# Kernel optimization log

Hardware: AMD Instinct MI355X
Metric: run time of the kernel (lower is better)

## Reference

```python
import math
import jax, jax.numpy as jnp
import numpy as np

HEADS = 20
NV = 6  # num_views


def _sdpa(q, k, v):
    # q,k,v: (B, H, Lq/Lk, D)
    d = q.shape[-1]
    scores = jnp.einsum('bhqd,bhkd->bhqk', q, k) * (1.0 / math.sqrt(d))
    return jnp.einsum('bhqk,bhkd->bhqd', jax.nn.softmax(scores, axis=-1), v)


def setup_inputs() -> dict:
    key = jax.random.key(0)
    ks = jax.random.split(key, 16)
    C = 1280
    bs, seq = 6, 1024
    w = 1.0 / math.sqrt(C)
    inp = {
        'hidden_states': jax.random.normal(ks[0], (bs, seq, C), jnp.float32),
        'ref_hidden_states': jax.random.normal(ks[1], (bs, seq, C), jnp.float32),
        'Wq': jax.random.normal(ks[2], (C, C), jnp.float32) * w,
        'Wk': jax.random.normal(ks[3], (C, C), jnp.float32) * w,
        'Wv': jax.random.normal(ks[4], (C, C), jnp.float32) * w,
        'Wout': jax.random.normal(ks[5], (C, C), jnp.float32) * w,
        'bout': jnp.zeros((C,), jnp.float32),
        'Wq_mv': jax.random.normal(ks[6], (C, C), jnp.float32) * w,
        'Wk_mv': jax.random.normal(ks[7], (C, C), jnp.float32) * w,
        'Wv_mv': jax.random.normal(ks[8], (C, C), jnp.float32) * w,
        'Wout_mv': jax.random.normal(ks[9], (C, C), jnp.float32) * w,
        'bout_mv': jnp.zeros((C,), jnp.float32),
        'Wq_ref': jax.random.normal(ks[10], (C, C), jnp.float32) * w,
        'Wk_ref': jax.random.normal(ks[11], (C, C), jnp.float32) * w,
        'Wv_ref': jax.random.normal(ks[12], (C, C), jnp.float32) * w,
        'Wout_ref': jax.random.normal(ks[13], (C, C), jnp.float32) * w,
        'bout_ref': jnp.zeros((C,), jnp.float32),
    }
    return inp


def reference(hidden_states, ref_hidden_states, Wq, Wk, Wv, Wout, bout,
              Wq_mv, Wk_mv, Wv_mv, Wout_mv, bout_mv,
              Wq_ref, Wk_ref, Wv_ref, Wout_ref, bout_ref):
    bs, seq, C = hidden_states.shape
    h = HEADS
    hd = Wq.shape[1] // h
    nv = NV
    b = bs // nv
    ih = iw = int(math.isqrt(seq))
    residual = hidden_states

    def split_heads(x):  # (bs, L, h*hd) -> (bs, h, L, hd)
        return x.reshape(bs, -1, h, hd).transpose(0, 2, 1, 3)

    def merge_heads(x):  # (bs, h, L, hd) -> (bs, L, h*hd)
        return x.transpose(0, 2, 1, 3).reshape(bs, -1, h * hd)

    # ---- base self-attention ----
    out = _sdpa(split_heads(hidden_states @ Wq),
                split_heads(hidden_states @ Wk),
                split_heads(hidden_states @ Wv))
    out = merge_heads(out) @ Wout + bout

    # ---- row-wise multi-view attention ----
    q_mv = (hidden_states @ Wq_mv).reshape(b, nv, ih, iw, h, hd)
    q_mv = q_mv.reshape(b * nv * ih, iw, h, hd).transpose(0, 2, 1, 3)  # (b*nv*ih, h, iw, hd)

    def mv_kv(x):
        # '(b nv)(ih iw) h c -> b ih (nv iw) h c', repeat_interleave(nv, dim=0)
        x = x.reshape(b, nv, ih, iw, h, hd).transpose(0, 2, 1, 3, 4, 5)
        x = x.reshape(b, ih, nv * iw, h, hd)
        x = jnp.repeat(x, nv, axis=0)  # (b*nv, ih, nv*iw, h, hd)
        return x.reshape(b * nv * ih, nv * iw, h, hd).transpose(0, 2, 1, 3)

    k_mv = mv_kv((hidden_states @ Wk_mv).reshape(bs, seq, h, hd).reshape(bs, seq, h * hd))
    v_mv = mv_kv((hidden_states @ Wv_mv))
    o_mv = _sdpa(q_mv, k_mv, v_mv)  # (b*nv*ih, h, iw, hd)
    # '(b nv ih) h iw c -> (b nv)(ih iw)(h c)'
    o_mv = o_mv.reshape(b, nv, ih, h, iw, hd).transpose(0, 1, 2, 4, 3, 5).reshape(bs, seq, h * hd)
    o_mv = o_mv @ Wout_mv + bout_mv

    # ---- reference image cross-attention ----
    o_ref = _sdpa(split_heads(hidden_states @ Wq_ref),
                  split_heads(ref_hidden_states @ Wk_ref),
                  split_heads(ref_hidden_states @ Wv_ref))
    o_ref = merge_heads(o_ref) @ Wout_ref + bout_ref

    mv_scale = 1.0
    ref_scale = 1.0
    return out + o_mv * mv_scale + o_ref * ref_scale + residual
```

## Files before the change

kernel.cpp:

```cpp
#include <hip/hip_runtime.h>
#include <hip/hip_bf16.h>


typedef __bf16 bf16;
typedef __bf16 bf16x8 __attribute__((ext_vector_type(8)));
typedef float f32x4 __attribute__((ext_vector_type(4)));

#define LOG2E 1.44269504088896340f

__device__ __forceinline__ unsigned pk2(float a, float b){
  unsigned short x = __builtin_bit_cast(unsigned short, (bf16)a);
  unsigned short y = __builtin_bit_cast(unsigned short, (bf16)b);
  return (unsigned)x | ((unsigned)y << 16);
}

__device__ __forceinline__ void glds16(const void* g, void* l){
  __builtin_amdgcn_global_load_lds((const __attribute__((address_space(1))) void*)g,
                                   (__attribute__((address_space(3))) void*)l, 16, 0, 0);
}

__global__ void __launch_bounds__(256) k_conv(const float* __restrict__ h,
                                              const float* __restrict__ r,
                                              bf16* __restrict__ xb, bf16* __restrict__ rb)
{
  size_t i = (size_t)blockIdx.x*256 + threadIdx.x;
  float4 a = ((const float4*)h)[i];
  uint2 u; u.x = pk2(a.x, a.y); u.y = pk2(a.z, a.w);
  ((uint2*)xb)[i] = u;
  float4 b = ((const float4*)r)[i];
  uint2 v; v.x = pk2(b.x, b.y); v.y = pk2(b.z, b.w);
  ((uint2*)rb)[i] = v;
}

struct W12 { const float* p[12]; };

__global__ void __launch_bounds__(256) k_wt(W12 srcs, bf16* __restrict__ wt_qkv,
                                            bf16* __restrict__ wt_ref, bf16* __restrict__ wt_out)
{
  int z = blockIdx.z;
  const float* src = srcs.p[z];
  float scale = (z==0 || z==3 || z==6) ? 0.125f : 1.0f;
  bf16* dst; int ldd;
  if (z < 7)      { dst = wt_qkv + (size_t)z*1280*1280; ldd = 1280; }
  else if (z < 9) { dst = wt_ref + (size_t)(z-7)*1280*1280; ldd = 1280; }
  else            { dst = wt_out + (size_t)(z-9)*1280; ldd = 3840; }

  __shared__ float tile[32][33];
  int tx = threadIdx.x & 31, ty = threadIdx.x >> 5;
  int r0 = blockIdx.y*32, c0 = blockIdx.x*32;
  #pragma unroll
  for (int i=0;i<32;i+=8)
    tile[ty+i][tx] = src[(size_t)(r0+ty+i)*1280 + c0+tx] * scale;
  __syncthreads();
  #pragma unroll
  for (int i=0;i<32;i+=8)
    dst[(size_t)(c0+ty+i)*ldd + r0+tx] = (bf16)tile[tx][ty+i];
}

template<int EPI>
__global__ void __launch_bounds__(256) k_gemm(const bf16* __restrict__ A, const bf16* __restrict__ BT,
            int K, int lda, int ldb,
            bf16* __restrict__ Crm, int ldc,
            bf16* __restrict__ VT1, bf16* __restrict__ VT2,
            const float* __restrict__ resid,
            const float* __restrict__ b0, const float* __restrict__ b1, const float* __restrict__ b2,
            float* __restrict__ outF)
{
  __shared__ bf16 As[128*64];
  __shared__ bf16 Bs[128*64];
  const int tid = threadIdx.x;
  const int w = tid >> 6, l = tid & 63;
  const int c = l & 15, g = l >> 4;
  const int m0 = blockIdx.y * 128, n0 = blockIdx.x * 128;
  const int wr = (w >> 1) * 64, wc = (w & 1) * 64;

  f32x4 acc[4][4];
  #pragma unroll
  for (int i=0;i<4;i++)
    #pragma unroll
    for (int j=0;j<4;j++) acc[i][j] = (f32x4){0.f,0.f,0.f,0.f};

  for (int k0 = 0; k0 < K; k0 += 64){
    __syncthreads();
    #pragma unroll
    for (int j=0;j<4;j++){
      int chunk = j*256 + tid;
      int row = chunk >> 3, cc = chunk & 7;
      int sc8 = ((cc ^ (row & 7)) << 3);
      glds16(A  + (size_t)(m0+row)*lda + k0 + sc8, (char*)As + ((size_t)(j*256 + (w<<6)) << 4));
      glds16(BT + (size_t)(n0+row)*ldb + k0 + sc8, (char*)Bs + ((size_t)(j*256 + (w<<6)) << 4));
    }
    __syncthreads();
    #pragma unroll
    for (int kk=0;kk<2;kk++){
      bf16x8 af[4], bfr[4];
      #pragma unroll
      for (int m=0;m<4;m++){
        int row = wr + m*16 + c;
        af[m] = *(const bf16x8*)((const char*)As + row*128 + ((((kk<<2)+g) ^ (row&7)) << 4));
      }
      #pragma unroll
      for (int n=0;n<4;n++){
        int row = wc + n*16 + c;
        bfr[n] = *(const bf16x8*)((const char*)Bs + row*128 + ((((kk<<2)+g) ^ (row&7)) << 4));
      }
      #pragma unroll
      for (int m=0;m<4;m++)
        #pragma unroll
        for (int n=0;n<4;n++)
          acc[m][n] = __builtin_amdgcn_mfma_f32_16x16x32_bf16(af[m], bfr[n], acc[m][n], 0,0,0);
    }
  }

  if (EPI == 2){
    #pragma unroll
    for (int nf=0;nf<4;nf++){
      int col = n0 + wc + nf*16 + c;
      float bias = b0[col] + b1[col] + b2[col];
      #pragma unroll
      for (int mf=0;mf<4;mf++)
        #pragma unroll
        for (int r=0;r<4;r++){
          int row = m0 + wr + mf*16 + (g<<2) + r;
          size_t idx = (size_t)row*1280 + col;
          outF[idx] = acc[mf][nf][r] + bias + resid[idx];
        }
    }
    return;
  }

  int reg = n0 / 1280;
  bool vt = (EPI==0) ? (reg==2 || reg==5) : (reg==1);
  if (!vt){
    int colbase = (EPI==0) ? (n0 - ((reg>=3)?1280:0) - ((reg>=6)?1280:0)) : n0;
    #pragma unroll
    for (int mf=0;mf<4;mf++)
      #pragma unroll
      for (int nf=0;nf<4;nf++)
        #pragma unroll
        for (int r=0;r<4;r++){
          int row = m0 + wr + mf*16 + (g<<2) + r;
          Crm[(size_t)row*ldc + colbase + wc + nf*16 + c] = (bf16)acc[mf][nf][r];
        }
  } else {
    bf16* vdst; int cm0; bool mv = false;
    if (EPI==0){
      if (reg==2){ vdst = VT1; cm0 = n0 - 2560; }
      else       { vdst = VT2; cm0 = n0 - 6400; mv = true; }
    } else       { vdst = VT1; cm0 = n0 - 1280; }
    #pragma unroll
    for (int nf=0;nf<4;nf++){
      int cm = cm0 + wc + nf*16 + c;
      int hh = cm >> 6, dd = cm & 63;
      #pragma unroll
      for (int mf=0;mf<4;mf++){
        int tok0 = m0 + wr + mf*16 + (g<<2);
        size_t addr;
        if (mv) addr = ((size_t)(hh*64 + dd))*6144 + tok0;
        else    addr = ((size_t)(((tok0>>10)*20 + hh)*64 + dd))*1024 + (size_t)(tok0 & 1023);
        uint2 v; v.x = pk2(acc[mf][nf][0], acc[mf][nf][1]); v.y = pk2(acc[mf][nf][2], acc[mf][nf][3]);
        *(uint2*)((char*)vdst + addr*2) = v;
      }
    }
  }
}

template<int MODE>
__global__ void __launch_bounds__(256) k_flash(const bf16* __restrict__ qkv5, const bf16* __restrict__ kref,
              const bf16* __restrict__ vt_base, const bf16* __restrict__ vt_mv,
              const bf16* __restrict__ vt_ref, bf16* __restrict__ outcat)
{
  __shared__ bf16 Ks[64*64];
  __shared__ bf16 VTs[64*64];
  __shared__ bf16 Pl[128*64];
  __shared__ float scl[128];
  __shared__ float lsum[128];

  const int tid = threadIdx.x;
  const int w = tid >> 6, l = tid & 63;
  const int c = l & 15, g = l >> 4;
  const int qt = blockIdx.x, grp = blockIdx.y;

  int hh, ldk, bidx = 0, iv = 0, NKT, Lq, ocol;
  const bf16 *Qb, *Kb, *Vb;
  if (MODE==0){
    bidx = grp/20; hh = grp%20;
    Qb = qkv5 + (size_t)hh*64;
    Kb = qkv5 + 1280 + (size_t)hh*64; ldk = 6400;
    Vb = vt_base + ((size_t)(bidx*20 + hh)*64)*1024;
    NKT = 16; Lq = 1024; ocol = hh*64;
  } else if (MODE==1){
    iv = grp/20; hh = grp%20;
    Qb = qkv5 + 2560 + (size_t)hh*64;
    Kb = qkv5 + 3840 + (size_t)hh*64; ldk = 6400;
    Vb = vt_mv + ((size_t)hh*64)*6144;
    NKT = 3; Lq = 192; ocol = 1280 + hh*64;
  } else {
    bidx = grp/20; hh = grp%20;
    Qb = qkv5 + 5120 + (size_t)hh*64;
    Kb = kref + (size_t)hh*64; ldk = 1280;
    Vb = vt_ref + ((size_t)(bidx*20 + hh)*64)*1024;
    NKT = 16; Lq = 1024; ocol = 2560 + hh*64;
  }

  bf16x8 qf[2][2];
  #pragma unroll
  for (int nf=0;nf<2;nf++){
    int qa = qt*128 + w*32 + nf*16 + c;
    if (qa > Lq-1) qa = Lq-1;
    int tq = (MODE==1) ? (((qa>>5)<<10) + iv*32 + (qa&31)) : ((bidx<<10) + qa);
    #pragma unroll
    for (int kk=0;kk<2;kk++)
      qf[nf][kk] = *(const bf16x8*)(Qb + (size_t)tq*6400 + kk*32 + g*8);
  }

  float mrow[2] = {-1e30f, -1e30f};
  float lrow[2] = {0.f, 0.f};
  f32x4 oacc[2][4];
  #pragma unroll
  for (int i=0;i<2;i++)
    #pragma unroll
    for (int j=0;j<4;j++) oacc[i][j] = (f32x4){0.f,0.f,0.f,0.f};

  for (int kt=0; kt<NKT; ++kt){
    __syncthreads();
    #pragma unroll
    for (int j=0;j<2;j++){
      int lc = j*256 + tid;
      int row = lc >> 3, cc = lc & 7;
      int sc8 = ((cc ^ (row&7)) << 3);
      int ka = kt*64 + row;
      int tk = (MODE==1) ? (((ka>>5)<<10) + iv*32 + (ka&31)) : ((bidx<<10) + ka);
      glds16(Kb + (size_t)tk*ldk + sc8, (char*)Ks + ((size_t)(j*256 + (w<<6))<<4));
    }
    #pragma unroll
    for (int j=0;j<2;j++){
      int lc = j*256 + tid;
      int dd = lc >> 3, cc = lc & 7;
      int k8 = kt*64 + ((cc ^ (dd&7)) << 3);
      const bf16* src;
      if (MODE==1) src = Vb + (size_t)dd*6144 + ((k8>>5)<<10) + iv*32 + (k8&31);
      else         src = Vb + (size_t)dd*1024 + k8;
      glds16(src, (char*)VTs + ((size_t)(j*256 + (w<<6))<<4));
    }
    __syncthreads();

    f32x4 st[4][2];
    #pragma unroll
    for (int m=0;m<4;m++)
      #pragma unroll
      for (int nf=0;nf<2;nf++) st[m][nf] = (f32x4){0.f,0.f,0.f,0.f};
    #pragma unroll
    for (int kk=0;kk<2;kk++){
      bf16x8 kf[4];
      #pragma unroll
      for (int m=0;m<4;m++){
        int row = m*16 + c;
        kf[m] = *(const bf16x8*)((const char*)Ks + row*128 + ((((kk<<2)+g)^(row&7))<<4));
      }
      #pragma unroll
      for (int m=0;m<4;m++)
        #pragma unroll
        for (int nf=0;nf<2;nf++)
          st[m][nf] = __builtin_amdgcn_mfma_f32_16x16x32_bf16(kf[m], qf[nf][kk], st[m][nf], 0,0,0);
    }

    #pragma unroll
    for (int nf=0;nf<2;nf++){
      float pm = st[0][nf][0];
      #pragma unroll
      for (int m=0;m<4;m++)
        #pragma unroll
        for (int r=0;r<4;r++) pm = fmaxf(pm, st[m][nf][r]);
      pm = fmaxf(pm, __shfl_xor(pm, 16));
      pm = fmaxf(pm, __shfl_xor(pm, 32));
      float mnew = fmaxf(mrow[nf], pm);
      float sc = exp2f((mrow[nf] - mnew) * LOG2E);
      float ps = 0.f;
      int qlds = w*32 + nf*16 + c;
      #pragma unroll
      for (int m=0;m<4;m++){
        float p0 = exp2f((st[m][nf][0]-mnew)*LOG2E);
        float p1 = exp2f((st[m][nf][1]-mnew)*LOG2E);
        float p2 = exp2f((st[m][nf][2]-mnew)*LOG2E);
        float p3 = exp2f((st[m][nf][3]-mnew)*LOG2E);
        ps += p0+p1+p2+p3;
        uint2 pv; pv.x = pk2(p0,p1); pv.y = pk2(p2,p3);
        int ci = ((m*2 + (g>>1)) ^ (qlds&7));
        *(uint2*)((char*)Pl + qlds*128 + (ci<<4) + ((g&1)<<3)) = pv;
      }
      ps += __shfl_xor(ps, 16);
      ps += __shfl_xor(ps, 32);
      lrow[nf] = lrow[nf]*sc + ps;
      mrow[nf] = mnew;
      scl[qlds] = sc;
    }
    #pragma unroll
    for (int mf=0;mf<2;mf++)
      #pragma unroll
      for (int r=0;r<4;r++){
        float s = scl[w*32 + mf*16 + (g<<2) + r];
        #pragma unroll
        for (int nd=0;nd<4;nd++) oacc[mf][nd][r] *= s;
      }
    #pragma unroll
    for (int ks=0;ks<2;ks++){
      bf16x8 pf[2], vf[4];
      #pragma unroll
      for (int mf=0;mf<2;mf++){
        int q = w*32 + mf*16 + c;
        pf[mf] = *(const bf16x8*)((const char*)Pl + q*128 + ((((ks<<2)+g)^(q&7))<<4));
      }
      #pragma unroll
      for (int nd=0;nd<4;nd++){
        int row = nd*16 + c;
        vf[nd] = *(const bf16x8*)((const char*)VTs + row*128 + ((((ks<<2)+g)^(row&7))<<4));
      }
      #pragma unroll
      for (int mf=0;mf<2;mf++)
        #pragma unroll
        for (int nd=0;nd<4;nd++)
          oacc[mf][nd] = __builtin_amdgcn_mfma_f32_16x16x32_bf16(pf[mf], vf[nd], oacc[mf][nd], 0,0,0);
    }
  }

  #pragma unroll
  for (int nf=0;nf<2;nf++) lsum[w*32 + nf*16 + c] = lrow[nf];
  #pragma unroll
  for (int mf=0;mf<2;mf++)
    #pragma unroll
    for (int r=0;r<4;r++){
      int qloc = w*32 + mf*16 + (g<<2) + r;
      float inv = 1.f / lsum[qloc];
      int qa = qt*128 + qloc;
      if (qa < Lq){
        int tq = (MODE==1) ? (((qa>>5)<<10) + iv*32 + (qa&31)) : ((bidx<<10) + qa);
        #pragma unroll
        for (int nd=0;nd<4;nd++)
          outcat[(size_t)tq*3840 + ocol + nd*16 + c] = (bf16)(oacc[mf][nd][r] * inv);
      }
    }
}

extern "C" void kernel_launch(void* const* d_in, const int* in_sizes, int n_in,
                              void* d_out, int out_size, void* d_ws, size_t ws_size,
                              hipStream_t stream)
{
  (void)in_sizes; (void)n_in; (void)out_size; (void)ws_size;
  const float* hs  = (const float*)d_in[0];
  const float* rhs = (const float*)d_in[1];
  const float* bq  = (const float*)d_in[6];
  const float* bm  = (const float*)d_in[11];
  const float* br  = (const float*)d_in[16];

  char* ws = (char*)d_ws;
  size_t off = 0;
  auto alloc = [&](size_t bytes){ size_t a = off; off += (bytes + 255) & ~(size_t)255; return a; };
  size_t oXBF   = alloc((size_t)6144*1280*2);
  size_t oRBF   = alloc((size_t)6144*1280*2);
  size_t oWTQKV = alloc((size_t)8960*1280*2);
  size_t oWTREF = alloc((size_t)2560*1280*2);
  size_t oWTOUT = alloc((size_t)1280*3840*2);
  size_t oQKV5  = alloc((size_t)6144*6400*2);
  size_t oKREF  = alloc((size_t)6144*1280*2);
  size_t oVTB   = alloc((size_t)6*20*64*1024*2);
  size_t oVTM   = alloc((size_t)20*64*6144*2);
  size_t oVTR   = alloc((size_t)6*20*64*1024*2);
  size_t oOUT   = oXBF;

  bf16* XBF   = (bf16*)(ws + oXBF);
  bf16* RBF   = (bf16*)(ws + oRBF);
  bf16* WTQKV = (bf16*)(ws + oWTQKV);
  bf16* WTREF = (bf16*)(ws + oWTREF);
  bf16* WTOUT = (bf16*)(ws + oWTOUT);
  bf16* QKV5  = (bf16*)(ws + oQKV5);
  bf16* KREF  = (bf16*)(ws + oKREF);
  bf16* VTB   = (bf16*)(ws + oVTB);
  bf16* VTM   = (bf16*)(ws + oVTM);
  bf16* VTR   = (bf16*)(ws + oVTR);
  bf16* OUTC  = (bf16*)(ws + oOUT);

  k_conv<<<7680, 256, 0, stream>>>(hs, rhs, XBF, RBF);

  W12 wsrc;
  wsrc.p[0]=(const float*)d_in[2];  wsrc.p[1]=(const float*)d_in[3];  wsrc.p[2]=(const float*)d_in[4];
  wsrc.p[3]=(const float*)d_in[7];  wsrc.p[4]=(const float*)d_in[8];  wsrc.p[5]=(const float*)d_in[9];
  wsrc.p[6]=(const float*)d_in[12]; wsrc.p[7]=(const float*)d_in[13]; wsrc.p[8]=(const float*)d_in[14];
  wsrc.p[9]=(const float*)d_in[5];  wsrc.p[10]=(const float*)d_in[10]; wsrc.p[11]=(const float*)d_in[15];
  k_wt<<<dim3(40,40,12), 256, 0, stream>>>(wsrc, WTQKV, WTREF, WTOUT);

  k_gemm<0><<<dim3(70,48), 256, 0, stream>>>(XBF, WTQKV, 1280, 1280, 1280,
      QKV5, 6400, VTB, VTM, nullptr, nullptr, nullptr, nullptr, nullptr);
  k_gemm<1><<<dim3(20,48), 256, 0, stream>>>(RBF, WTREF, 1280, 1280, 1280,
      KREF, 1280, VTR, nullptr, nullptr, nullptr, nullptr, nullptr, nullptr);

  k_flash<0><<<dim3(8,120), 256, 0, stream>>>(QKV5, KREF, VTB, VTM, VTR, OUTC);
  k_flash<1><<<dim3(2,640), 256, 0, stream>>>(QKV5, KREF, VTB, VTM, VTR, OUTC);
  k_flash<2><<<dim3(8,120), 256, 0, stream>>>(QKV5, KREF, VTB, VTM, VTR, OUTC);

  k_gemm<2><<<dim3(10,48), 256, 0, stream>>>(OUTC, WTOUT, 3840, 3840, 3840,
      nullptr, 0, nullptr, nullptr, hs, bq, bm, br, (float*)d_out);
}
```

Before: 726.9 us.

## Rewrite projection GEMMs with 256x256 tiles and double-buffered LDS pipeline

```diff
diff --git a/kernel.cpp b/kernel.cpp
--- a/kernel.cpp
+++ b/kernel.cpp
@@ -57,76 +57,113 @@
     dst[(size_t)(c0+ty+i)*ldd + r0+tx] = (bf16)tile[tx][ty+i];
 }
 
+
+template<int MQ, int NQ>
+__device__ __forceinline__ void frag_load(const char* Ab, const char* Bb,
+          int wr, int wc, int c, int g, bf16x8 (&af)[4][2], bf16x8 (&bfr)[2][2])
+{
+  #pragma unroll
+  for (int mf=0;mf<4;mf++){
+    int row = wr + MQ*64 + mf*16 + c;
+    #pragma unroll
+    for (int kk=0;kk<2;kk++)
+      af[mf][kk] = *(const bf16x8*)(Ab + row*128 + ((((kk<<2)+g)^(row&7))<<4));
+  }
+  #pragma unroll
+  for (int nf=0;nf<2;nf++){
+    int row = wc + NQ*32 + nf*16 + c;
+    #pragma unroll
+    for (int kk=0;kk<2;kk++)
+      bfr[nf][kk] = *(const bf16x8*)(Bb + row*128 + ((((kk<<2)+g)^(row&7))<<4));
+  }
+}
+
+template<int MQ, int NQ>
+__device__ __forceinline__ void frag_mfma(f32x4 (&acc)[8][4], bf16x8 (&af)[4][2], bf16x8 (&bfr)[2][2])
+{
+  __builtin_amdgcn_s_setprio(1);
+  #pragma unroll
+  for (int kk=0;kk<2;kk++)
+    #pragma unroll
+    for (int mf=0;mf<4;mf++)
+      #pragma unroll
+      for (int nf=0;nf<2;nf++)
+        acc[MQ*4+mf][NQ*2+nf] = __builtin_amdgcn_mfma_f32_16x16x32_bf16(
+            af[mf][kk], bfr[nf][kk], acc[MQ*4+mf][NQ*2+nf], 0,0,0);
+  __builtin_amdgcn_s_setprio(0);
+}
+
+#define BAR()    __builtin_amdgcn_s_barrier()
+#define VMC(N)   asm volatile("s_waitcnt vmcnt(" #N ")" ::: "memory")
+
 template<int EPI>
-__global__ void __launch_bounds__(256) k_gemm(const bf16* __restrict__ A, const bf16* __restrict__ BT,
+__global__ void __launch_bounds__(512,2) k_gemm8(const bf16* __restrict__ A, const bf16* __restrict__ BT,
             int K, int lda, int ldb,
             bf16* __restrict__ Crm, int ldc,
-            bf16* __restrict__ VT1, bf16* __restrict__ VT2,
-            const float* __restrict__ resid,
-            const float* __restrict__ b0, const float* __restrict__ b1, const float* __restrict__ b2,
-            float* __restrict__ outF)
-{
-  __shared__ bf16 As[128*64];
-  __shared__ bf16 Bs[128*64];
+            bf16* __restrict__ VT1, bf16* __restrict__ VT2)
+{
+  __shared__ __align__(16) char lds[131072];
   const int tid = threadIdx.x;
   const int w = tid >> 6, l = tid & 63;
   const int c = l & 15, g = l >> 4;
-  const int m0 = blockIdx.y * 128, n0 = blockIdx.x * 128;
-  const int wr = (w >> 1) * 64, wc = (w & 1) * 64;
-
-  f32x4 acc[4][4];
-  #pragma unroll
-  for (int i=0;i<4;i++)
+  const int m0 = blockIdx.y * 256, n0 = blockIdx.x * 256;
+  const int wr = (w >> 2) * 128, wc = (w & 3) * 64;
+  const int qh = l >> 3, cc = l & 7;
+
+  f32x4 acc[8][4];
+  #pragma unroll
+  for (int i=0;i<8;i++)
     #pragma unroll
     for (int j=0;j<4;j++) acc[i][j] = (f32x4){0.f,0.f,0.f,0.f};
-
-  for (int k0 = 0; k0 < K; k0 += 64){
-    __syncthreads();
-    #pragma unroll
-    for (int j=0;j<4;j++){
-      int chunk = j*256 + tid;
-      int row = chunk >> 3, cc = chunk & 7;
-      int sc8 = ((cc ^ (row & 7)) << 3);
-      glds16(A  + (size_t)(m0+row)*lda + k0 + sc8, (char*)As + ((size_t)(j*256 + (w<<6)) << 4));
-      glds16(BT + (size_t)(n0+row)*ldb + k0 + sc8, (char*)Bs + ((size_t)(j*256 + (w<<6)) << 4));
-    }
-    __syncthreads();
-    #pragma unroll
-    for (int kk=0;kk<2;kk++){
-      bf16x8 af[4], bfr[4];
-      #pragma unroll
-      for (int m=0;m<4;m++){
-        int row = wr + m*16 + c;
-        af[m] = *(const bf16x8*)((const char*)As + row*128 + ((((kk<<2)+g) ^ (row&7)) << 4));
-      }
-      #pragma unroll
-      for (int n=0;n<4;n++){
-        int row = wc + n*16 + c;
-        bfr[n] = *(const bf16x8*)((const char*)Bs + row*128 + ((((kk<<2)+g) ^ (row&7)) << 4));
-      }
-      #pragma unroll
-      for (int m=0;m<4;m++)
-        #pragma unroll
-        for (int n=0;n<4;n++)
-          acc[m][n] = __builtin_amdgcn_mfma_f32_16x16x32_bf16(af[m], bfr[n], acc[m][n], 0,0,0);
-    }
-  }
-
-  if (EPI == 2){
-    #pragma unroll
-    for (int nf=0;nf<4;nf++){
-      int col = n0 + wc + nf*16 + c;
-      float bias = b0[col] + b1[col] + b2[col];
-      #pragma unroll
-      for (int mf=0;mf<4;mf++)
-        #pragma unroll
-        for (int r=0;r<4;r++){
-          int row = m0 + wr + mf*16 + (g<<2) + r;
-          size_t idx = (size_t)row*1280 + col;
-          outF[idx] = acc[mf][nf][r] + bias + resid[idx];
-        }
-    }
-    return;
+  bf16x8 af[4][2], bfr[2][2];
+
+  auto stA = [&](int db, int k0, int Y){
+    char* base = lds + db*32768;
+    #pragma unroll
+    for (int i=0;i<2;i++){
+      int qr0 = w*16 + i*8;
+      int ar0 = (qr0 & 63) + ((qr0>>6)<<7) + (Y<<6);
+      int row = ar0 + qh;
+      glds16(A + (size_t)(m0+row)*lda + k0 + ((cc ^ (row&7))<<3), base + (ar0<<7));
+    }
+  };
+  auto stB = [&](int db, int k0, int Y){
+    char* base = lds + 65536 + db*32768;
+    #pragma unroll
+    for (int i=0;i<2;i++){
+      int qr0 = w*16 + i*8;
+      int br0 = (qr0 & 31) + ((qr0>>5)<<6) + (Y<<5);
+      int row = br0 + qh;
+      glds16(BT + (size_t)(n0+row)*ldb + k0 + ((cc ^ (row&7))<<3), base + (br0<<7));
+    }
+  };
+
+  stA(0,0,0); stB(0,0,0); stB(0,0,1); stA(0,0,1);
+  VMC(4);
+  BAR();
+
+  const int NT = K >> 6;
+  for (int j = 0; j < NT-1; ++j){
+    const int db = j & 1, k1 = (j+1) << 6;
+    const char* Ab = lds + db*32768;
+    const char* Bb = lds + 65536 + db*32768;
+    frag_load<0,0>(Ab,Bb,wr,wc,c,g,af,bfr); stA(db^1,k1,0);
+    BAR(); frag_mfma<0,0>(acc,af,bfr); VMC(4); BAR();
+    frag_load<0,1>(Ab,Bb,wr,wc,c,g,af,bfr); stB(db^1,k1,0);
+    BAR(); frag_mfma<0,1>(acc,af,bfr); VMC(4); BAR();
+    frag_load<1,0>(Ab,Bb,wr,wc,c,g,af,bfr); stB(db^1,k1,1);
+    BAR(); frag_mfma<1,0>(acc,af,bfr); BAR();
+    frag_load<1,1>(Ab,Bb,wr,wc,c,g,af,bfr); stA(db^1,k1,1);
+    BAR(); frag_mfma<1,1>(acc,af,bfr); VMC(4); BAR();
+  }
+  {
+    const int db = (NT-1) & 1;
+    const char* Ab = lds + db*32768;
+    const char* Bb = lds + 65536 + db*32768;
+    frag_load<0,0>(Ab,Bb,wr,wc,c,g,af,bfr); BAR(); frag_mfma<0,0>(acc,af,bfr); VMC(2); BAR();
+    frag_load<0,1>(Ab,Bb,wr,wc,c,g,af,bfr); BAR(); frag_mfma<0,1>(acc,af,bfr); VMC(0); BAR();
+    frag_load<1,0>(Ab,Bb,wr,wc,c,g,af,bfr); BAR(); frag_mfma<1,0>(acc,af,bfr); BAR();
+    frag_load<1,1>(Ab,Bb,wr,wc,c,g,af,bfr); BAR(); frag_mfma<1,1>(acc,af,bfr);
   }
 
   int reg = n0 / 1280;
@@ -134,7 +171,7 @@
   if (!vt){
     int colbase = (EPI==0) ? (n0 - ((reg>=3)?1280:0) - ((reg>=6)?1280:0)) : n0;
     #pragma unroll
-    for (int mf=0;mf<4;mf++)
+    for (int mf=0;mf<8;mf++)
       #pragma unroll
       for (int nf=0;nf<4;nf++)
         #pragma unroll
@@ -153,7 +190,7 @@
       int cm = cm0 + wc + nf*16 + c;
       int hh = cm >> 6, dd = cm & 63;
       #pragma unroll
-      for (int mf=0;mf<4;mf++){
+      for (int mf=0;mf<8;mf++){
         int tok0 = m0 + wr + mf*16 + (g<<2);
         size_t addr;
         if (mv) addr = ((size_t)(hh*64 + dd))*6144 + tok0;
@@ -162,6 +199,73 @@
         *(uint2*)((char*)vdst + addr*2) = v;
       }
     }
+  }
+}
+
+__global__ void __launch_bounds__(256) k_gemm_out(const bf16* __restrict__ A, const bf16* __restrict__ BT,
+            int K, int lda, int ldb,
+            const float* __restrict__ resid,
+            const float* __restrict__ b0, const float* __restrict__ b1, const float* __restrict__ b2,
+            float* __restrict__ outF)
+{
+  __shared__ bf16 As[128*64];
+  __shared__ bf16 Bs[128*64];
+  const int tid = threadIdx.x;
+  const int w = tid >> 6, l = tid & 63;
+  const int c = l & 15, g = l >> 4;
+  const int m0 = blockIdx.y * 128, n0 = blockIdx.x * 128;
+  const int wr = (w >> 1) * 64, wc = (w & 1) * 64;
+
+  f32x4 acc[4][4];
+  #pragma unroll
+  for (int i=0;i<4;i++)
+    #pragma unroll
+    for (int j=0;j<4;j++) acc[i][j] = (f32x4){0.f,0.f,0.f,0.f};
+
+  for (int k0 = 0; k0 < K; k0 += 64){
+    __syncthreads();
+    #pragma unroll
+    for (int j=0;j<4;j++){
+      int chunk = j*256 + tid;
+      int row = chunk >> 3, cc = chunk & 7;
+      int sc8 = ((cc ^ (row & 7)) << 3);
+      glds16(A  + (size_t)(m0+row)*lda + k0 + sc8, (char*)As + ((size_t)(j*256 + (w<<6)) << 4));
+      glds16(BT + (size_t)(n0+row)*ldb + k0 + sc8, (char*)Bs + ((size_t)(j*256 + (w<<6)) << 4));
+    }
+    __syncthreads();
+    #pragma unroll
+    for (int kk=0;kk<2;kk++){
+      bf16x8 af[4], bfr[4];
+      #pragma unroll
+      for (int m=0;m<4;m++){
+        int row = wr + m*16 + c;
+        af[m] = *(const bf16x8*)((const char*)As + row*128 + ((((kk<<2)+g) ^ (row&7)) << 4));
+      }
+      #pragma unroll
+      for (int n=0;n<4;n++){
+        int row = wc + n*16 + c;
+        bfr[n] = *(const bf16x8*)((const char*)Bs + row*128 + ((((kk<<2)+g) ^ (row&7)) << 4));
+      }
+      #pragma unroll
+      for (int m=0;m<4;m++)
+        #pragma unroll
+        for (int n=0;n<4;n++)
+          acc[m][n] = __builtin_amdgcn_mfma_f32_16x16x32_bf16(af[m], bfr[n], acc[m][n], 0,0,0);
+    }
+  }
+
+  #pragma unroll
+  for (int nf=0;nf<4;nf++){
+    int col = n0 + wc + nf*16 + c;
+    float bias = b0[col] + b1[col] + b2[col];
+    #pragma unroll
+    for (int mf=0;mf<4;mf++)
+      #pragma unroll
+      for (int r=0;r<4;r++){
+        int row = m0 + wr + mf*16 + (g<<2) + r;
+        size_t idx = (size_t)row*1280 + col;
+        outF[idx] = acc[mf][nf][r] + bias + resid[idx];
+      }
   }
 }
 
@@ -389,15 +493,15 @@
   wsrc.p[9]=(const float*)d_in[5];  wsrc.p[10]=(const float*)d_in[10]; wsrc.p[11]=(const float*)d_in[15];
   k_wt<<<dim3(40,40,12), 256, 0, stream>>>(wsrc, WTQKV, WTREF, WTOUT);
 
-  k_gemm<0><<<dim3(70,48), 256, 0, stream>>>(XBF, WTQKV, 1280, 1280, 1280,
-      QKV5, 6400, VTB, VTM, nullptr, nullptr, nullptr, nullptr, nullptr);
-  k_gemm<1><<<dim3(20,48), 256, 0, stream>>>(RBF, WTREF, 1280, 1280, 1280,
-      KREF, 1280, VTR, nullptr, nullptr, nullptr, nullptr, nullptr, nullptr);
+  k_gemm8<0><<<dim3(35,24), 512, 0, stream>>>(XBF, WTQKV, 1280, 1280, 1280,
+      QKV5, 6400, VTB, VTM);
+  k_gemm8<1><<<dim3(10,24), 512, 0, stream>>>(RBF, WTREF, 1280, 1280, 1280,
+      KREF, 1280, VTR, nullptr);
 
   k_flash<0><<<dim3(8,120), 256, 0, stream>>>(QKV5, KREF, VTB, VTM, VTR, OUTC);
   k_flash<1><<<dim3(2,640), 256, 0, stream>>>(QKV5, KREF, VTB, VTM, VTR, OUTC);
   k_flash<2><<<dim3(8,120), 256, 0, stream>>>(QKV5, KREF, VTB, VTM, VTR, OUTC);
 
-  k_gemm<2><<<dim3(10,48), 256, 0, stream>>>(OUTC, WTOUT, 3840, 3840, 3840,
-      nullptr, 0, nullptr, nullptr, hs, bq, bm, br, (float*)d_out);
-}
+  k_gemm_out<<<dim3(10,48), 256, 0, stream>>>(OUTC, WTOUT, 3840, 3840, 3840,
+      hs, bq, bm, br, (float*)d_out);
+}
```

New measurement: 714.3 us. About the same (-1.7%).
